# Performance work log

Hardware: AMD Instinct MI355X
Metric: run time of the kernel (lower is better)

The kernel has to match this reference:

```python
import jax, jax.numpy as jnp
import numpy as np

B, S, D = 4, 2048, 1024

def setup_inputs() -> dict:
    key = jax.random.key(0)
    ks = jax.random.split(key, 7)
    sc = 1.0 / np.sqrt(D)
    return {
        "x": jax.random.normal(ks[0], (B, S, D), dtype=jnp.float32),
        "Wq": jax.random.normal(ks[1], (D, D), dtype=jnp.float32) * sc,
        "bq": jax.random.normal(ks[2], (D,), dtype=jnp.float32) * 0.01,
        "Wk": jax.random.normal(ks[3], (D, D), dtype=jnp.float32) * sc,
        "bk": jax.random.normal(ks[4], (D,), dtype=jnp.float32) * 0.01,
        "Wv": jax.random.normal(ks[5], (D, D), dtype=jnp.float32) * sc,
        "bv": jax.random.normal(ks[6], (D,), dtype=jnp.float32) * 0.01,
    }

def reference(x, Wq, bq, Wk, bk, Wv, bv):
    # q, k, v: [B, S, D] projections (torch Linear: x @ W^T + b; here W stored as [in, out])
    q = jnp.einsum("bsd,df->bsf", x, Wq) + bq
    k = jnp.einsum("bsd,df->bsf", x, Wk) + bk
    v = jnp.einsum("bsd,df->bsf", x, Wv) + bv
    dim = x.shape[-1]
    # scores: [B, S, S], scaled by sqrt(full d_model) as in the source
    scores = jnp.einsum("bqd,bkd->bqk", q, k) / jnp.sqrt(jnp.float32(dim)).astype(x.dtype)
    attn = jax.nn.softmax(scores, axis=-1)
    return jnp.einsum("bqk,bkd->bqd", attn, v)
```

## Files before the change

kernel.cpp:

```cpp
#include <hip/hip_runtime.h>
#include <hip/hip_bf16.h>

typedef __attribute__((ext_vector_type(8))) short bf16x8;
typedef __attribute__((ext_vector_type(4))) float f32x4;
typedef unsigned short u16;

__device__ __forceinline__ u16 f2bf(float f) {
  unsigned int u = __builtin_bit_cast(unsigned int, f);
  u += 0x7fffu + ((u >> 16) & 1u);
  return (u16)(u >> 16);
}
__device__ __forceinline__ float bf2f(unsigned int h) {
  unsigned int u = h << 16;
  return __builtin_bit_cast(float, u);
}

__device__ __forceinline__ void gload_lds16(const void* g, void* l) {
  __builtin_amdgcn_global_load_lds(
      (const __attribute__((address_space(1))) void*)g,
      (__attribute__((address_space(3))) void*)l, 16, 0, 0);
}

#define VMC(N) asm volatile("s_waitcnt vmcnt(%0)" ::"n"(N) : "memory")

template <int BM, int EPI>
__global__ __launch_bounds__(512, 2) void gemm8p(
    const u16* __restrict__ Abase, const u16* __restrict__ Btbase,
    const float* __restrict__ bq, const float* __restrict__ bk,
    const float* __restrict__ bv, void* __restrict__ out0,
    void* __restrict__ out1, void* __restrict__ out2, int Kd, int ldc,
    long long sAz, long long sBz, long long sCz) {
  constexpr int AHALF = BM * 64;
  constexpr int BHALF = 16384;
  constexpr int BUFSZ = 2 * AHALF + 2 * BHALF;
  constexpr int AU_ = AHALF / 8192;
  constexpr int MF = BM / 64;
  __shared__ char lds[2 * BUFSZ];

  const int tid = threadIdx.x;
  const int w = tid >> 6, l = tid & 63;
  const int wr = w >> 2, wc = w & 3;
  const int lq = l >> 4, lr = l & 15;
  const int bm = blockIdx.y * BM, bn = blockIdx.x * 256;
  const int z = blockIdx.z;
  const u16* A = Abase + (size_t)z * sAz;
  const u16* Bt = Btbase + (size_t)z * sBz;
  const int NT = Kd >> 6;

  const int kbp = ((tid & 7) ^ ((tid >> 3) & 7)) * 8;
  const int drow = tid >> 3;
  const u16* gAr[2][AU_];
  const u16* gBr[2][2];
#pragma unroll
  for (int h = 0; h < 2; ++h) {
#pragma unroll
    for (int u = 0; u < AU_; ++u)
      gAr[h][u] =
          A + (size_t)(bm + h * (BM / 2) + u * 64 + drow) * Kd + kbp;
#pragma unroll
    for (int u = 0; u < 2; ++u)
      gBr[h][u] = Bt + (size_t)(bn + h * 128 + u * 64 + drow) * Kd + kbp;
  }

  auto stageA = [&](int buf, int h, int t) {
    char* d = lds + buf * BUFSZ + h * AHALF + tid * 16;
#pragma unroll
    for (int u = 0; u < AU_; ++u) gload_lds16(gAr[h][u] + t * 64, d + u * 8192);
  };
  auto stageB = [&](int buf, int h, int t) {
    char* d = lds + buf * BUFSZ + 2 * AHALF + h * BHALF + tid * 16;
#pragma unroll
    for (int u = 0; u < 2; ++u) gload_lds16(gBr[h][u] + t * 64, d + u * 8192);
  };

  const int rA = wr * (BM / 4) + lr;
  const int rB = wc * 32 + lr;
  int aoff[2], boff[2];
#pragma unroll
  for (int kh = 0; kh < 2; ++kh) {
    aoff[kh] = rA * 128 + (((kh * 4 + lq) ^ (rA & 7)) << 4);
    boff[kh] = rB * 128 + (((kh * 4 + lq) ^ (rB & 7)) << 4);
  }

  f32x4 acc[2][MF][2][2] = {};
  bf16x8 a[2][MF];
  bf16x8 bb[2][2][2];

  constexpr int NQ0 = (BM == 256) ? 4 : 2;
  constexpr int NQ1 = (BM == 256) ? 4 : 3;
  constexpr int NQ2 = 4;
  constexpr int NQ3 = (BM == 256) ? 4 : 3;

#define RD_A(MQ)                                                            \
  {                                                                         \
    const char* ab = lds + buf * BUFSZ + (MQ)*AHALF;                        \
    _Pragma("unroll") for (int kh = 0; kh < 2; ++kh)                        \
        _Pragma("unroll") for (int mf = 0; mf < MF; ++mf) a[kh][mf] =       \
            *(const bf16x8*)(ab + aoff[kh] + mf * 2048);                    \
  }
#define RD_B(NQ)                                                            \
  {                                                                         \
    const char* bbp = lds + buf * BUFSZ + 2 * AHALF + (NQ)*BHALF;           \
    _Pragma("unroll") for (int kh = 0; kh < 2; ++kh)                        \
        _Pragma("unroll") for (int nf = 0; nf < 2; ++nf) bb[NQ][kh][nf] =   \
            *(const bf16x8*)(bbp + boff[kh] + nf * 2048);                   \
  }
#define MMAQ(MQ, NQ)                                                        \
  {                                                                         \
    __builtin_amdgcn_s_setprio(1);                                          \
    _Pragma("unroll") for (int kh = 0; kh < 2; ++kh)                        \
        _Pragma("unroll") for (int mf = 0; mf < MF; ++mf)                   \
            _Pragma("unroll") for (int nf = 0; nf < 2; ++nf)                \
                acc[MQ][mf][NQ][nf] = __builtin_amdgcn_mfma_f32_16x16x32_bf16( \
                    a[kh][mf], bb[NQ][kh][nf], acc[MQ][mf][NQ][nf], 0, 0, 0);  \
    __builtin_amdgcn_s_setprio(0);                                          \
  }

  stageA(0, 0, 0);
  stageB(0, 0, 0);
  stageB(0, 1, 0);
  stageA(0, 1, 0);
  stageA(1, 0, 1);
  VMC(NQ0);
  __builtin_amdgcn_s_barrier();

  for (int t = 0; t < NT; ++t) {
    const int buf = t & 1, sb = buf ^ 1;
    VMC(NQ0);
    RD_A(0);
    RD_B(0);
    if (t + 1 < NT) stageB(sb, 0, t + 1);
    if constexpr (BM == 256)
      asm volatile("s_waitcnt lgkmcnt(8)" ::: "memory");
    __builtin_amdgcn_s_barrier();
    MMAQ(0, 0);
    __builtin_amdgcn_s_barrier();
    VMC(NQ1);
    RD_B(1);
    if (t + 1 < NT) stageB(sb, 1, t + 1);
    __builtin_amdgcn_s_barrier();
    MMAQ(0, 1);
    __builtin_amdgcn_s_barrier();
    VMC(NQ2);
    RD_A(1);
    if (t + 1 < NT) stageA(sb, 1, t + 1);
    __builtin_amdgcn_s_barrier();
    MMAQ(1, 1);
    __builtin_amdgcn_s_barrier();
    VMC(NQ3);
    if (t + 2 < NT) stageA(buf, 0, t + 2);
    __builtin_amdgcn_s_barrier();
    MMAQ(1, 0);
    __builtin_amdgcn_s_barrier();
  }

  if constexpr (EPI == 0) {
    const int mat = bn >> 10;
    const float sc = (mat == 0) ? 0.03125f : 1.0f;
    const float* bias = (mat == 0) ? bq : (mat == 1 ? bk : bv);
    u16* Q = (u16*)out0;
    u16* K = (u16*)out1;
    u16* V = (u16*)out2;
#pragma unroll
    for (int nq = 0; nq < 2; ++nq)
#pragma unroll
      for (int nf = 0; nf < 2; ++nf) {
        const int oc = ((bn + wc * 32 + nq * 128 + nf * 16 + lr) & 1023);
        const float bb2 = bias[oc];
#pragma unroll
        for (int mq = 0; mq < 2; ++mq)
#pragma unroll
          for (int mf = 0; mf < MF; ++mf) {
            const int row =
                bm + wr * (BM / 4) + mq * (BM / 2) + mf * 16 + lq * 4;
            if (mat < 2) {
              u16* dst = (mat == 0) ? Q : K;
#pragma unroll
              for (int e = 0; e < 4; ++e)
                dst[(size_t)(row + e) * 1024 + oc] =
                    f2bf((acc[mq][mf][nq][nf][e] + bb2) * sc);
            } else {
              const int bz = row >> 11, sdx = row & 2047;
              ushort4 pk;
              pk.x = f2bf(acc[mq][mf][nq][nf][0] + bb2);
              pk.y = f2bf(acc[mq][mf][nq][nf][1] + bb2);
              pk.z = f2bf(acc[mq][mf][nq][nf][2] + bb2);
              pk.w = f2bf(acc[mq][mf][nq][nf][3] + bb2);
              *(ushort4*)&V[((size_t)bz * 1024 + oc) * 2048 + sdx] = pk;
            }
          }
      }
  } else if constexpr (EPI == 2) {
    u16* C = (u16*)out0 + (size_t)z * sCz;
#pragma unroll
    for (int nq = 0; nq < 2; ++nq)
#pragma unroll
      for (int nf = 0; nf < 2; ++nf) {
        const int col = bn + wc * 32 + nq * 128 + nf * 16 + lr;
#pragma unroll
        for (int mq = 0; mq < 2; ++mq)
#pragma unroll
          for (int mf = 0; mf < MF; ++mf) {
            const int row =
                bm + wr * (BM / 4) + mq * (BM / 2) + mf * 16 + lq * 4;
#pragma unroll
            for (int e = 0; e < 4; ++e)
              C[(size_t)(row + e) * ldc + col] = f2bf(acc[mq][mf][nq][nf][e]);
          }
      }
  } else {
    float* C = (float*)out0 + (size_t)z * sCz;
#pragma unroll
    for (int nq = 0; nq < 2; ++nq)
#pragma unroll
      for (int nf = 0; nf < 2; ++nf) {
        const int col = bn + wc * 32 + nq * 128 + nf * 16 + lr;
#pragma unroll
        for (int mq = 0; mq < 2; ++mq)
#pragma unroll
          for (int mf = 0; mf < MF; ++mf) {
            const int row =
                bm + wr * (BM / 4) + mq * (BM / 2) + mf * 16 + lq * 4;
#pragma unroll
            for (int e = 0; e < 4; ++e)
              C[(size_t)(row + e) * ldc + col] = acc[mq][mf][nq][nf][e];
          }
      }
  }
#undef RD_A
#undef RD_B
#undef MMAQ
}

__global__ __launch_bounds__(256) void cvt_x(const float* __restrict__ in,
                                             u16* __restrict__ out) {
  const int i = blockIdx.x * 256 + threadIdx.x;
  const float4 v = ((const float4*)in)[i];
  ushort4 o;
  o.x = f2bf(v.x);
  o.y = f2bf(v.y);
  o.z = f2bf(v.z);
  o.w = f2bf(v.w);
  ((ushort4*)out)[i] = o;
}

__global__ void cvt_wt(const float* __restrict__ Wq,
                       const float* __restrict__ Wk,
                       const float* __restrict__ Wv, u16* __restrict__ Wt) {
  __shared__ float s[32][33];
  const float* W = blockIdx.z == 0 ? Wq : (blockIdx.z == 1 ? Wk : Wv);
  u16* O = Wt + (size_t)blockIdx.z * 1048576;
  const int k0 = blockIdx.y * 32, n0 = blockIdx.x * 32;
  s[threadIdx.y][threadIdx.x] =
      W[(size_t)(k0 + threadIdx.y) * 1024 + n0 + threadIdx.x];
  __syncthreads();
  O[(size_t)(n0 + threadIdx.y) * 1024 + k0 + threadIdx.x] =
      f2bf(s[threadIdx.x][threadIdx.y]);
}

__global__ __launch_bounds__(256) void softmax_rows(u16* __restrict__ SP) {
  const size_t base = ((size_t)blockIdx.y * 2048 + blockIdx.x) * 2048;
  u16* p = SP + base;
  const int t = threadIdx.x;
  __shared__ float red[4];

  uint4 u = ((const uint4*)p)[t];
  unsigned int uu[4] = {u.x, u.y, u.z, u.w};
  float f[8];
#pragma unroll
  for (int j = 0; j < 4; ++j) {
    f[2 * j] = bf2f(uu[j] & 0xffffu);
    f[2 * j + 1] = __builtin_bit_cast(float, uu[j] & 0xffff0000u);
  }
  float mx = f[0];
#pragma unroll
  for (int i = 1; i < 8; ++i) mx = fmaxf(mx, f[i]);
#pragma unroll
  for (int o = 32; o; o >>= 1) mx = fmaxf(mx, __shfl_xor(mx, o, 64));
  if ((t & 63) == 0) red[t >> 6] = mx;
  __syncthreads();
  mx = fmaxf(fmaxf(red[0], red[1]), fmaxf(red[2], red[3]));
  __syncthreads();

  float e[8];
  float sum = 0.f;
#pragma unroll
  for (int i = 0; i < 8; ++i) {
    e[i] = __expf(f[i] - mx);
    sum += e[i];
  }
#pragma unroll
  for (int o = 32; o; o >>= 1) sum += __shfl_xor(sum, o, 64);
  if ((t & 63) == 0) red[t >> 6] = sum;
  __syncthreads();
  sum = red[0] + red[1] + red[2] + red[3];
  const float inv = 1.0f / sum;

  uint4 ov;
  unsigned int w0[4];
#pragma unroll
  for (int j = 0; j < 4; ++j) {
    unsigned int lo = f2bf(e[2 * j] * inv);
    unsigned int hi = f2bf(e[2 * j + 1] * inv);
    w0[j] = lo | (hi << 16);
  }
  ov.x = w0[0];
  ov.y = w0[1];
  ov.z = w0[2];
  ov.w = w0[3];
  ((uint4*)p)[t] = ov;
}

extern "C" void kernel_launch(void* const* d_in, const int* in_sizes, int n_in,
                              void* d_out, int out_size, void* d_ws,
                              size_t ws_size, hipStream_t stream) {
  const float* x = (const float*)d_in[0];
  const float* Wq = (const float*)d_in[1];
  const float* bq = (const float*)d_in[2];
  const float* Wk = (const float*)d_in[3];
  const float* bk = (const float*)d_in[4];
  const float* Wv = (const float*)d_in[5];
  const float* bv = (const float*)d_in[6];
  float* out = (float*)d_out;
  char* ws = (char*)d_ws;

  u16* xb = (u16*)ws;
  u16* Wt = (u16*)(ws + 16777216);
  u16* Qb = (u16*)(ws + 23068672);
  u16* Kb = Qb + 8388608;
  u16* Vt = Kb + 8388608;
  u16* SP = Vt + 8388608;

  cvt_x<<<8192, 256, 0, stream>>>(x, xb);
  cvt_wt<<<dim3(32, 32, 3), dim3(32, 32), 0, stream>>>(Wq, Wk, Wv, Wt);

  gemm8p<256, 0><<<dim3(12, 32, 1), 512, 0, stream>>>(
      xb, Wt, bq, bk, bv, Qb, Kb, Vt, 1024, 0, 0, 0, 0);

  gemm8p<256, 2><<<dim3(8, 8, 4), 512, 0, stream>>>(
      Qb, Kb, nullptr, nullptr, nullptr, SP, nullptr, nullptr, 1024, 2048,
      2097152LL, 2097152LL, 4194304LL);

  softmax_rows<<<dim3(2048, 4), 256, 0, stream>>>(SP);

  gemm8p<128, 3><<<dim3(4, 16, 4), 512, 0, stream>>>(
      SP, Vt, nullptr, nullptr, nullptr, out, nullptr, nullptr, 2048, 1024,
      4194304LL, 2097152LL, 2097152LL);
}
```

Before: 179.3 us.

## Restructure GEMM pipelines: unrolled double-buffer schedule and triple-buffered B for PV GEMM

The 256x256 GEMM kernel's main loop is unrolled by two k-tiles with explicit buffer indices. It adds LDS waitcnt fences and moves the global prefetches to new points in the schedule, so loads for both buffers can overlap the MFMA quadrants. The attention-times-V GEMM gets a dedicated 128x256 kernel. That kernel double-buffers A, triple-buffers B in LDS, and runs a two-phase loop per k-tile. The bigger LDS footprint and the added lgkmcnt(0) waits before each MFMA block may limit occupancy or serialize LDS reads.

```diff
diff --git a/kernel.cpp b/kernel.cpp
--- a/kernel.cpp
+++ b/kernel.cpp
@@ -21,59 +21,56 @@
       (__attribute__((address_space(3))) void*)l, 16, 0, 0);
 }
 
+#define BAR() __builtin_amdgcn_s_barrier()
+#define LGKM0() asm volatile("s_waitcnt lgkmcnt(0)" ::: "memory")
+#define LGKM8() asm volatile("s_waitcnt lgkmcnt(8)" ::: "memory")
 #define VMC(N) asm volatile("s_waitcnt vmcnt(%0)" ::"n"(N) : "memory")
 
-template <int BM, int EPI>
-__global__ __launch_bounds__(512, 2) void gemm8p(
+template <int EPI>
+__global__ __launch_bounds__(512, 2) void gemm8x(
     const u16* __restrict__ Abase, const u16* __restrict__ Btbase,
     const float* __restrict__ bq, const float* __restrict__ bk,
     const float* __restrict__ bv, void* __restrict__ out0,
     void* __restrict__ out1, void* __restrict__ out2, int Kd, int ldc,
     long long sAz, long long sBz, long long sCz) {
-  constexpr int AHALF = BM * 64;
-  constexpr int BHALF = 16384;
-  constexpr int BUFSZ = 2 * AHALF + 2 * BHALF;
-  constexpr int AU_ = AHALF / 8192;
-  constexpr int MF = BM / 64;
+  constexpr int HSZ = 16384;
+  constexpr int BUFSZ = 4 * HSZ;
   __shared__ char lds[2 * BUFSZ];
 
   const int tid = threadIdx.x;
   const int w = tid >> 6, l = tid & 63;
   const int wr = w >> 2, wc = w & 3;
   const int lq = l >> 4, lr = l & 15;
-  const int bm = blockIdx.y * BM, bn = blockIdx.x * 256;
+  const int bm = blockIdx.y * 256, bn = blockIdx.x * 256;
   const int z = blockIdx.z;
   const u16* A = Abase + (size_t)z * sAz;
   const u16* Bt = Btbase + (size_t)z * sBz;
-  const int NT = Kd >> 6;
+  const int NTk = Kd >> 6, NI = NTk >> 1;
 
   const int kbp = ((tid & 7) ^ ((tid >> 3) & 7)) * 8;
   const int drow = tid >> 3;
-  const u16* gAr[2][AU_];
-  const u16* gBr[2][2];
-#pragma unroll
-  for (int h = 0; h < 2; ++h) {
-#pragma unroll
-    for (int u = 0; u < AU_; ++u)
-      gAr[h][u] =
-          A + (size_t)(bm + h * (BM / 2) + u * 64 + drow) * Kd + kbp;
-#pragma unroll
-    for (int u = 0; u < 2; ++u)
-      gBr[h][u] = Bt + (size_t)(bn + h * 128 + u * 64 + drow) * Kd + kbp;
-  }
-
-  auto stageA = [&](int buf, int h, int t) {
-    char* d = lds + buf * BUFSZ + h * AHALF + tid * 16;
-#pragma unroll
-    for (int u = 0; u < AU_; ++u) gload_lds16(gAr[h][u] + t * 64, d + u * 8192);
-  };
-  auto stageB = [&](int buf, int h, int t) {
-    char* d = lds + buf * BUFSZ + 2 * AHALF + h * BHALF + tid * 16;
-#pragma unroll
-    for (int u = 0; u < 2; ++u) gload_lds16(gBr[h][u] + t * 64, d + u * 8192);
-  };
-
-  const int rA = wr * (BM / 4) + lr;
+  const u16* gA[2][2];
+  const u16* gB[2][2];
+#pragma unroll
+  for (int h = 0; h < 2; ++h)
+#pragma unroll
+    for (int u = 0; u < 2; ++u) {
+      gA[h][u] = A + (size_t)(bm + h * 128 + u * 64 + drow) * Kd + kbp;
+      gB[h][u] = Bt + (size_t)(bn + h * 128 + u * 64 + drow) * Kd + kbp;
+    }
+
+  auto stageA = [&](int buf, int h, int kt) {
+    char* d = lds + buf * BUFSZ + h * HSZ + tid * 16;
+    gload_lds16(gA[h][0] + kt * 64, d);
+    gload_lds16(gA[h][1] + kt * 64, d + 8192);
+  };
+  auto stageB = [&](int buf, int h, int kt) {
+    char* d = lds + buf * BUFSZ + (2 + h) * HSZ + tid * 16;
+    gload_lds16(gB[h][0] + kt * 64, d);
+    gload_lds16(gB[h][1] + kt * 64, d + 8192);
+  };
+
+  const int rA = wr * 64 + lr;
   const int rB = wc * 32 + lr;
   int aoff[2], boff[2];
 #pragma unroll
@@ -82,38 +79,33 @@
     boff[kh] = rB * 128 + (((kh * 4 + lq) ^ (rB & 7)) << 4);
   }
 
-  f32x4 acc[2][MF][2][2] = {};
-  bf16x8 a[2][MF];
+  f32x4 acc[2][4][2][2] = {};
+  bf16x8 a[2][4];
   bf16x8 bb[2][2][2];
 
-  constexpr int NQ0 = (BM == 256) ? 4 : 2;
-  constexpr int NQ1 = (BM == 256) ? 4 : 3;
-  constexpr int NQ2 = 4;
-  constexpr int NQ3 = (BM == 256) ? 4 : 3;
-
-#define RD_A(MQ)                                                            \
+#define RD_A(BUF, MQ)                                                       \
   {                                                                         \
-    const char* ab = lds + buf * BUFSZ + (MQ)*AHALF;                        \
+    const char* p_ = lds + (BUF)*BUFSZ + (MQ)*HSZ;                          \
     _Pragma("unroll") for (int kh = 0; kh < 2; ++kh)                        \
-        _Pragma("unroll") for (int mf = 0; mf < MF; ++mf) a[kh][mf] =       \
-            *(const bf16x8*)(ab + aoff[kh] + mf * 2048);                    \
-  }
-#define RD_B(NQ)                                                            \
+        _Pragma("unroll") for (int mf = 0; mf < 4; ++mf) a[kh][mf] =        \
+            *(const bf16x8*)(p_ + aoff[kh] + mf * 2048);                    \
+  }
+#define RD_B(BUF, NQ)                                                       \
   {                                                                         \
-    const char* bbp = lds + buf * BUFSZ + 2 * AHALF + (NQ)*BHALF;           \
+    const char* p_ = lds + (BUF)*BUFSZ + (2 + (NQ)) * HSZ;                  \
     _Pragma("unroll") for (int kh = 0; kh < 2; ++kh)                        \
         _Pragma("unroll") for (int nf = 0; nf < 2; ++nf) bb[NQ][kh][nf] =   \
-            *(const bf16x8*)(bbp + boff[kh] + nf * 2048);                   \
-  }
-#define MMAQ(MQ, NQ)                                                        \
-  {                                                                         \
-    __builtin_amdgcn_s_setprio(1);                                          \
-    _Pragma("unroll") for (int kh = 0; kh < 2; ++kh)                        \
-        _Pragma("unroll") for (int mf = 0; mf < MF; ++mf)                   \
-            _Pragma("unroll") for (int nf = 0; nf < 2; ++nf)                \
-                acc[MQ][mf][NQ][nf] = __builtin_amdgcn_mfma_f32_16x16x32_bf16( \
-                    a[kh][mf], bb[NQ][kh][nf], acc[MQ][mf][NQ][nf], 0, 0, 0);  \
-    __builtin_amdgcn_s_setprio(0);                                          \
+            *(const bf16x8*)(p_ + boff[kh] + nf * 2048);                    \
+  }
+#define MMAQ(MQ, NQ)                                                          \
+  {                                                                           \
+    __builtin_amdgcn_s_setprio(1);                                            \
+    _Pragma("unroll") for (int kh = 0; kh < 2; ++kh)                          \
+        _Pragma("unroll") for (int mf = 0; mf < 4; ++mf)                      \
+            _Pragma("unroll") for (int nf = 0; nf < 2; ++nf) acc[MQ][mf][NQ]  \
+                [nf] = __builtin_amdgcn_mfma_f32_16x16x32_bf16(               \
+                    a[kh][mf], bb[NQ][kh][nf], acc[MQ][mf][NQ][nf], 0, 0, 0); \
+    __builtin_amdgcn_s_setprio(0);                                            \
   }
 
   stageA(0, 0, 0);
@@ -121,37 +113,64 @@
   stageB(0, 1, 0);
   stageA(0, 1, 0);
   stageA(1, 0, 1);
-  VMC(NQ0);
-  __builtin_amdgcn_s_barrier();
-
-  for (int t = 0; t < NT; ++t) {
-    const int buf = t & 1, sb = buf ^ 1;
-    VMC(NQ0);
-    RD_A(0);
-    RD_B(0);
-    if (t + 1 < NT) stageB(sb, 0, t + 1);
-    if constexpr (BM == 256)
-      asm volatile("s_waitcnt lgkmcnt(8)" ::: "memory");
-    __builtin_amdgcn_s_barrier();
+  stageB(1, 0, 1);
+  stageB(1, 1, 1);
+  VMC(6);
+  BAR();
+
+  for (int i = 0; i < NI; ++i) {
+    const int kt1 = 2 * i + 1, ktn0 = 2 * i + 2, ktn1 = 2 * i + 3;
+    const bool s0 = ktn0 < NTk, s1 = ktn1 < NTk;
+    RD_A(0, 0);
+    RD_B(0, 0);
+    stageA(1, 1, kt1);
+    LGKM8();
+    BAR();
+    LGKM0();
     MMAQ(0, 0);
-    __builtin_amdgcn_s_barrier();
-    VMC(NQ1);
-    RD_B(1);
-    if (t + 1 < NT) stageB(sb, 1, t + 1);
-    __builtin_amdgcn_s_barrier();
+    BAR();
+    RD_B(0, 1);
+    if (s0) stageA(0, 0, ktn0);
+    BAR();
+    LGKM0();
     MMAQ(0, 1);
-    __builtin_amdgcn_s_barrier();
-    VMC(NQ2);
-    RD_A(1);
-    if (t + 1 < NT) stageA(sb, 1, t + 1);
-    __builtin_amdgcn_s_barrier();
+    BAR();
+    RD_A(0, 1);
+    if (s0) stageB(0, 0, ktn0);
+    BAR();
+    LGKM0();
     MMAQ(1, 1);
-    __builtin_amdgcn_s_barrier();
-    VMC(NQ3);
-    if (t + 2 < NT) stageA(buf, 0, t + 2);
-    __builtin_amdgcn_s_barrier();
+    BAR();
+    if (s0) stageB(0, 1, ktn0);
+    BAR();
     MMAQ(1, 0);
-    __builtin_amdgcn_s_barrier();
+    if (i + 1 < NI) VMC(6); else VMC(0);
+    BAR();
+    RD_A(1, 0);
+    RD_B(1, 0);
+    if (s0) stageA(0, 1, ktn0);
+    LGKM8();
+    BAR();
+    LGKM0();
+    MMAQ(0, 0);
+    BAR();
+    RD_B(1, 1);
+    if (s1) stageA(1, 0, ktn1);
+    BAR();
+    LGKM0();
+    MMAQ(0, 1);
+    BAR();
+    RD_A(1, 1);
+    if (s1) stageB(1, 0, ktn1);
+    BAR();
+    LGKM0();
+    MMAQ(1, 1);
+    BAR();
+    if (s1) stageB(1, 1, ktn1);
+    BAR();
+    MMAQ(1, 0);
+    VMC(6);
+    BAR();
   }
 
   if constexpr (EPI == 0) {
@@ -166,31 +185,30 @@
 #pragma unroll
       for (int nf = 0; nf < 2; ++nf) {
         const int oc = ((bn + wc * 32 + nq * 128 + nf * 16 + lr) & 1023);
-        const float bb2 = bias[oc];
+        const float bv2 = bias[oc];
 #pragma unroll
         for (int mq = 0; mq < 2; ++mq)
 #pragma unroll
-          for (int mf = 0; mf < MF; ++mf) {
-            const int row =
-                bm + wr * (BM / 4) + mq * (BM / 2) + mf * 16 + lq * 4;
+          for (int mf = 0; mf < 4; ++mf) {
+            const int row = bm + wr * 64 + mq * 128 + mf * 16 + lq * 4;
             if (mat < 2) {
               u16* dst = (mat == 0) ? Q : K;
 #pragma unroll
               for (int e = 0; e < 4; ++e)
                 dst[(size_t)(row + e) * 1024 + oc] =
-                    f2bf((acc[mq][mf][nq][nf][e] + bb2) * sc);
+                    f2bf((acc[mq][mf][nq][nf][e] + bv2) * sc);
             } else {
               const int bz = row >> 11, sdx = row & 2047;
               ushort4 pk;
-              pk.x = f2bf(acc[mq][mf][nq][nf][0] + bb2);
-              pk.y = f2bf(acc[mq][mf][nq][nf][1] + bb2);
-              pk.z = f2bf(acc[mq][mf][nq][nf][2] + bb2);
-              pk.w = f2bf(acc[mq][mf][nq][nf][3] + bb2);
+              pk.x = f2bf(acc[mq][mf][nq][nf][0] + bv2);
+              pk.y = f2bf(acc[mq][mf][nq][nf][1] + bv2);
+              pk.z = f2bf(acc[mq][mf][nq][nf][2] + bv2);
+              pk.w = f2bf(acc[mq][mf][nq][nf][3] + bv2);
               *(ushort4*)&V[((size_t)bz * 1024 + oc) * 2048 + sdx] = pk;
             }
           }
       }
-  } else if constexpr (EPI == 2) {
+  } else {
     u16* C = (u16*)out0 + (size_t)z * sCz;
 #pragma unroll
     for (int nq = 0; nq < 2; ++nq)
@@ -200,36 +218,141 @@
 #pragma unroll
         for (int mq = 0; mq < 2; ++mq)
 #pragma unroll
-          for (int mf = 0; mf < MF; ++mf) {
-            const int row =
-                bm + wr * (BM / 4) + mq * (BM / 2) + mf * 16 + lq * 4;
+          for (int mf = 0; mf < 4; ++mf) {
+            const int row = bm + wr * 64 + mq * 128 + mf * 16 + lq * 4;
 #pragma unroll
             for (int e = 0; e < 4; ++e)
               C[(size_t)(row + e) * ldc + col] = f2bf(acc[mq][mf][nq][nf][e]);
           }
       }
-  } else {
-    float* C = (float*)out0 + (size_t)z * sCz;
-#pragma unroll
-    for (int nq = 0; nq < 2; ++nq)
-#pragma unroll
-      for (int nf = 0; nf < 2; ++nf) {
-        const int col = bn + wc * 32 + nq * 128 + nf * 16 + lr;
-#pragma unroll
-        for (int mq = 0; mq < 2; ++mq)
-#pragma unroll
-          for (int mf = 0; mf < MF; ++mf) {
-            const int row =
-                bm + wr * (BM / 4) + mq * (BM / 2) + mf * 16 + lq * 4;
-#pragma unroll
-            for (int e = 0; e < 4; ++e)
-              C[(size_t)(row + e) * ldc + col] = acc[mq][mf][nq][nf][e];
-          }
-      }
   }
 #undef RD_A
 #undef RD_B
 #undef MMAQ
+}
+
+__global__ __launch_bounds__(512, 2) void gemm2v(
+    const u16* __restrict__ Abase, const u16* __restrict__ Btbase,
+    float* __restrict__ outp, int Kd, int ldc, long long sAz, long long sBz,
+    long long sCz) {
+  constexpr int ASZ = 16384;
+  constexpr int BSZ = 32768;
+  constexpr int BBASE = 2 * ASZ;
+  __shared__ char lds[2 * ASZ + 3 * BSZ];
+
+  const int tid = threadIdx.x;
+  const int w = tid >> 6, l = tid & 63;
+  const int wr = w >> 2, wc = w & 3;
+  const int lq = l >> 4, lr = l & 15;
+  const int bm = blockIdx.y * 128, bn = blockIdx.x * 256;
+  const int z = blockIdx.z;
+  const u16* A = Abase + (size_t)z * sAz;
+  const u16* Bt = Btbase + (size_t)z * sBz;
+  const int NT = Kd >> 6;
+
+  const int kbp = ((tid & 7) ^ ((tid >> 3) & 7)) * 8;
+  const int drow = tid >> 3;
+  const u16* gA[2];
+  const u16* gB[4];
+#pragma unroll
+  for (int u = 0; u < 2; ++u)
+    gA[u] = A + (size_t)(bm + u * 64 + drow) * Kd + kbp;
+#pragma unroll
+  for (int u = 0; u < 4; ++u)
+    gB[u] = Bt + (size_t)(bn + u * 64 + drow) * Kd + kbp;
+
+  auto stageA = [&](int kt) {
+    char* d = lds + (kt & 1) * ASZ + tid * 16;
+#pragma unroll
+    for (int u = 0; u < 2; ++u) gload_lds16(gA[u] + kt * 64, d + u * 8192);
+  };
+  auto stageB = [&](int kt) {
+    char* d = lds + BBASE + (kt % 3) * BSZ + tid * 16;
+#pragma unroll
+    for (int u = 0; u < 4; ++u) gload_lds16(gB[u] + kt * 64, d + u * 8192);
+  };
+
+  const int rA = wr * 64 + lr;
+  const int rB0 = wc * 64 + lr;
+  int aoff[2];
+#pragma unroll
+  for (int kh = 0; kh < 2; ++kh)
+    aoff[kh] = rA * 128 + (((kh * 4 + lq) ^ (rA & 7)) << 4);
+
+  f32x4 acc[4][2][2] = {};
+  bf16x8 a[2][4], b[2][2];
+
+  auto rdA = [&](int kt) {
+    const char* p = lds + (kt & 1) * ASZ;
+#pragma unroll
+    for (int kh = 0; kh < 2; ++kh)
+#pragma unroll
+      for (int mf = 0; mf < 4; ++mf)
+        a[kh][mf] = *(const bf16x8*)(p + aoff[kh] + mf * 2048);
+  };
+  auto rdB = [&](int kt, int nh) {
+    const char* p = lds + BBASE + (kt % 3) * BSZ;
+    const int rB = rB0 + nh * 32;
+#pragma unroll
+    for (int kh = 0; kh < 2; ++kh) {
+      const int o = rB * 128 + (((kh * 4 + lq) ^ (rB & 7)) << 4);
+#pragma unroll
+      for (int nf = 0; nf < 2; ++nf)
+        b[kh][nf] = *(const bf16x8*)(p + o + nf * 2048);
+    }
+  };
+  auto mma = [&](int nh) {
+    __builtin_amdgcn_s_setprio(1);
+#pragma unroll
+    for (int kh = 0; kh < 2; ++kh)
+#pragma unroll
+      for (int mf = 0; mf < 4; ++mf)
+#pragma unroll
+        for (int nf = 0; nf < 2; ++nf)
+          acc[mf][nh][nf] = __builtin_amdgcn_mfma_f32_16x16x32_bf16(
+              a[kh][mf], b[kh][nf], acc[mf][nh][nf], 0, 0, 0);
+    __builtin_amdgcn_s_setprio(0);
+  };
+
+  stageB(0);
+  stageA(0);
+  stageB(1);
+  stageA(1);
+  VMC(6);
+  BAR();
+
+  for (int t = 0; t < NT; ++t) {
+    rdA(t);
+    rdB(t, 0);
+    if (t + 2 < NT) stageB(t + 2);
+    LGKM8();
+    BAR();
+    LGKM0();
+    mma(0);
+    BAR();
+    rdB(t, 1);
+    if (t + 2 < NT) stageA(t + 2);
+    BAR();
+    LGKM0();
+    mma(1);
+    if (t + 3 <= NT) VMC(6); else VMC(0);
+    BAR();
+  }
+
+  float* C = outp + (size_t)z * sCz;
+#pragma unroll
+  for (int nh = 0; nh < 2; ++nh)
+#pragma unroll
+    for (int nf = 0; nf < 2; ++nf) {
+      const int col = bn + wc * 64 + nh * 32 + nf * 16 + lr;
+#pragma unroll
+      for (int mf = 0; mf < 4; ++mf) {
+        const int row = bm + wr * 64 + mf * 16 + lq * 4;
+#pragma unroll
+        for (int e = 0; e < 4; ++e)
+          C[(size_t)(row + e) * ldc + col] = acc[mf][nh][nf][e];
+      }
+    }
 }
 
 __global__ __launch_bounds__(256) void cvt_x(const float* __restrict__ in,
@@ -334,16 +457,15 @@
   cvt_x<<<8192, 256, 0, stream>>>(x, xb);
   cvt_wt<<<dim3(32, 32, 3), dim3(32, 32), 0, stream>>>(Wq, Wk, Wv, Wt);
 
-  gemm8p<256, 0><<<dim3(12, 32, 1), 512, 0, stream>>>(
+  gemm8x<0><<<dim3(12, 32, 1), 512, 0, stream>>>(
       xb, Wt, bq, bk, bv, Qb, Kb, Vt, 1024, 0, 0, 0, 0);
 
-  gemm8p<256, 2><<<dim3(8, 8, 4), 512, 0, stream>>>(
+  gemm8x<2><<<dim3(8, 8, 4), 512, 0, stream>>>(
       Qb, Kb, nullptr, nullptr, nullptr, SP, nullptr, nullptr, 1024, 2048,
       2097152LL, 2097152LL, 4194304LL);
 
   softmax_rows<<<dim3(2048, 4), 256, 0, stream>>>(SP);
 
-  gemm8p<128, 3><<<dim3(4, 16, 4), 512, 0, stream>>>(
-      SP, Vt, nullptr, nullptr, nullptr, out, nullptr, nullptr, 2048, 1024,
-      4194304LL, 2097152LL, 2097152LL);
-}
+  gemm2v<<<dim3(4, 16, 4), 512, 0, stream>>>(
+      SP, Vt, out, 2048, 1024, 4194304LL, 2097152LL, 2097152LL);
+}
```

Measured after the change: 181.1 us. About the same (+1.0%).
